# Kernel optimization log

Hardware: AMD Instinct MI355X
Metric: run time of the kernel (lower is better)

## Reference

```python
import jax, jax.numpy as jnp
import numpy as np

D_MODEL = 512
N_HEADS = 8
D_HEAD = D_MODEL // N_HEADS
B = 8
N = 1024
EPS = 1e-5  # torch LayerNorm default


def setup_inputs() -> dict:
    key = jax.random.key(0)
    ks = jax.random.split(key, 12)
    x = jax.random.normal(ks[0], (B, N, D_MODEL), dtype=jnp.float32)
    adj = (jax.random.uniform(ks[1], (B, N, N)) < 0.05).astype(jnp.float32)
    s = 1.0 / np.sqrt(D_MODEL)
    def lin(kw, kb):
        W = jax.random.uniform(kw, (D_MODEL, D_MODEL), minval=-s, maxval=s, dtype=jnp.float32)
        b = jax.random.uniform(kb, (D_MODEL,), minval=-s, maxval=s, dtype=jnp.float32)
        return W, b
    Wq, bq = lin(ks[2], ks[3])
    Wk, bk = lin(ks[4], ks[5])
    Wv, bv = lin(ks[6], ks[7])
    Wo, bo = lin(ks[8], ks[9])
    gamma = jnp.ones((D_MODEL,), dtype=jnp.float32)
    beta = jnp.zeros((D_MODEL,), dtype=jnp.float32)
    return {"x": x, "adj": adj, "Wq": Wq, "bq": bq, "Wk": Wk, "bk": bk,
            "Wv": Wv, "bv": bv, "Wo": Wo, "bo": bo, "gamma": gamma, "beta": beta}


def reference(x, adj, Wq, bq, Wk, bk, Wv, bv, Wo, bo, gamma, beta):
    Bsz, n, _ = x.shape
    # QKV projections -> [b, h, n, d]
    def proj(W, b):
        y = x @ W.T + b
        return y.reshape(Bsz, n, N_HEADS, D_HEAD).transpose(0, 2, 1, 3)
    q, k, v = proj(Wq, bq), proj(Wk, bk), proj(Wv, bv)
    scores = jnp.einsum('bhqd,bhkd->bhqk', q, k) / np.sqrt(D_HEAD)
    # adjacency mask + self-loops, broadcast over heads
    mask = (adj + jnp.eye(n, dtype=adj.dtype)[None]) > 0  # [b, n, n]
    scores = jnp.where(mask[:, None], scores, -jnp.inf)
    attn = jax.nn.softmax(scores, axis=-1)  # dropout is identity in eval
    out = jnp.einsum('bhqk,bhkd->bhqd', attn, v)
    out = out.transpose(0, 2, 1, 3).reshape(Bsz, n, D_MODEL)
    out = out @ Wo.T + bo
    # residual + LayerNorm
    h = x + out
    mu = jnp.mean(h, axis=-1, keepdims=True)
    var = jnp.mean(jnp.square(h - mu), axis=-1, keepdims=True)
    return (h - mu) * jax.lax.rsqrt(var + EPS) * gamma + beta
```

## Files before the change

### kernel.cpp

```cpp
#include <hip/hip_runtime.h>

typedef __bf16 bf16;
typedef bf16 bf16x8 __attribute__((ext_vector_type(8)));
typedef bf16 bf16x4 __attribute__((ext_vector_type(4)));
typedef bf16 bf16x2 __attribute__((ext_vector_type(2)));
typedef float f32x4 __attribute__((ext_vector_type(4)));
typedef unsigned long long u64;

#define B_SZ 8
#define N_SEQ 1024
#define DMODEL 512
#define N_HEADS 8
#define D_HEAD 64
#define M_ROWS 8192

#define QSCALE 0.18033688011112042f

static constexpr size_t OFF_XB   = 0;
static constexpr size_t OFF_WQKV = (size_t)M_ROWS * DMODEL * 2;
static constexpr size_t OFF_WO   = OFF_WQKV + (size_t)1536 * 512 * 2;
static constexpr size_t OFF_BQKV = OFF_WO + (size_t)512 * 512 * 2;
static constexpr size_t OFF_Q    = OFF_BQKV + 1536 * 4;
static constexpr size_t OFF_K    = OFF_Q + (size_t)64 * 1024 * 64 * 2;
static constexpr size_t OFF_V    = OFF_K + (size_t)64 * 1024 * 64 * 2;
static constexpr size_t OFF_MASK = OFF_V + (size_t)64 * 1024 * 64 * 2;

#define PREP_X_BLK 4096
#define PREP_W_BLK 4102
#define PREP_M_BLK 32768

__device__ __forceinline__ f32x4 mfma16(bf16x8 a, bf16x8 b, f32x4 c) {
  return __builtin_amdgcn_mfma_f32_16x16x32_bf16(a, b, c, 0, 0, 0);
}

__device__ __forceinline__ int sidx(int row, int col) {
  return (row << 6) + (col ^ ((row & 7) << 3));
}

__device__ __forceinline__ void gload16(const void* g, void* l) {
  __builtin_amdgcn_global_load_lds(
      (const __attribute__((address_space(1))) void*)g,
      (__attribute__((address_space(3))) void*)l, 16, 0, 0);
}

__global__ void k_prep(const float* __restrict__ x, const float* __restrict__ adj,
                       const float* __restrict__ Wq, const float* __restrict__ Wk,
                       const float* __restrict__ Wv, const float* __restrict__ Wo,
                       const float* __restrict__ bq, const float* __restrict__ bk,
                       const float* __restrict__ bv,
                       bf16* __restrict__ xb, bf16* __restrict__ wqkv,
                       bf16* __restrict__ wo, float* __restrict__ bqkv,
                       u64* __restrict__ maskb) {
  int b = blockIdx.x;
  if (b < PREP_X_BLK) {
    int i = b * 256 + threadIdx.x;
    float4 v = reinterpret_cast<const float4*>(x)[i];
    bf16x4 o = { (bf16)v.x, (bf16)v.y, (bf16)v.z, (bf16)v.w };
    *reinterpret_cast<bf16x4*>(xb + (size_t)i * 4) = o;
  } else if (b < PREP_X_BLK + PREP_W_BLK) {
    int tid = (b - PREP_X_BLK) * 256 + threadIdx.x;
    if (tid < 1536 * 512) {
      int row = tid >> 9;
      const float* Wsrc = row < 512 ? Wq : row < 1024 ? Wk : Wv;
      wqkv[tid] = (bf16)Wsrc[((row & 511) << 9) | (tid & 511)];
    } else if (tid < 1536 * 512 + 512 * 512) {
      int t = tid - 1536 * 512;
      wo[t] = (bf16)Wo[t];
    } else if (tid < 1536 * 512 + 512 * 512 + 1536) {
      int t = tid - (1536 * 512 + 512 * 512);
      bqkv[t] = t < 512 ? bq[t] : t < 1024 ? bk[t - 512] : bv[t - 1024];
    }
  } else {
    int idx = (b - (PREP_X_BLK + PREP_W_BLK)) * 256 + threadIdx.x;
    int q = (idx >> 10) & 1023, k = idx & 1023;
    bool pred = (adj[idx] > 0.f) || (q == k);
    u64 bal = __ballot(pred);
    if ((threadIdx.x & 63) == 0) maskb[idx >> 6] = bal;
  }
}

__global__ __launch_bounds__(256) void k_gemm(const bf16* __restrict__ A,
    const bf16* __restrict__ W, int ncols, int mode,
    const float* __restrict__ bias, const float* __restrict__ xres,
    bf16* __restrict__ oq, bf16* __restrict__ okk, bf16* __restrict__ ov,
    bf16* __restrict__ oh) {
  __shared__ bf16 Al[128 * 64];
  __shared__ bf16 Bl[128 * 64];
  int nbx = ncols >> 7;
  int bx = blockIdx.x % nbx, by = blockIdx.x / nbx;
  int m0 = by << 7, n0 = bx << 7;
  int tid = threadIdx.x, lane = tid & 63, w = tid >> 6;
  int wr = (w >> 1) << 6, wc = (w & 1) << 6;
  int lrow = lane & 15, lg = lane >> 4, lko = lg * 8;
  int rl = lane >> 3;
  int csw = ((lane & 7) ^ rl) << 3;

  const bf16* Asrc = A + (size_t)(m0 + w * 32 + rl) * DMODEL + csw;
  const bf16* Wsrc = W + (size_t)(n0 + w * 32 + rl) * DMODEL + csw;
  bf16* Adst = &Al[(w * 4) * 512];
  bf16* Bdst = &Bl[(w * 4) * 512];

  f32x4 acc[4][4];
#pragma unroll
  for (int i = 0; i < 4; i++)
#pragma unroll
    for (int j = 0; j < 4; j++) acc[i][j] = f32x4{0.f, 0.f, 0.f, 0.f};

  for (int k0 = 0; k0 < DMODEL; k0 += 64) {
    __syncthreads();
#pragma unroll
    for (int i = 0; i < 4; i++) {
      gload16(Asrc + k0 + (size_t)i * 8 * DMODEL, Adst + i * 512);
      gload16(Wsrc + k0 + (size_t)i * 8 * DMODEL, Bdst + i * 512);
    }
    __syncthreads();

    bf16x8 afr[4][2], bfr[4][2];
#pragma unroll
    for (int i = 0; i < 4; i++) {
      afr[i][0] = *reinterpret_cast<const bf16x8*>(&Al[sidx(wr + i * 16 + lrow, lko)]);
      afr[i][1] = *reinterpret_cast<const bf16x8*>(&Al[sidx(wr + i * 16 + lrow, 32 + lko)]);
      bfr[i][0] = *reinterpret_cast<const bf16x8*>(&Bl[sidx(wc + i * 16 + lrow, lko)]);
      bfr[i][1] = *reinterpret_cast<const bf16x8*>(&Bl[sidx(wc + i * 16 + lrow, 32 + lko)]);
    }
#pragma unroll
    for (int i = 0; i < 4; i++)
#pragma unroll
      for (int j = 0; j < 4; j++) {
        acc[i][j] = mfma16(afr[i][0], bfr[j][0], acc[i][j]);
        acc[i][j] = mfma16(afr[i][1], bfr[j][1], acc[i][j]);
      }
  }

  int rbase = lg * 4;
  if (mode == 0) {
#pragma unroll
    for (int i = 0; i < 4; i++) {
      int row0 = m0 + wr + i * 16 + rbase;
#pragma unroll
      for (int j = 0; j < 4; j++) {
        int col = n0 + wc + j * 16 + lrow;
        int which = col >> 9, c2 = col & 511, hh = c2 >> 6, dd = c2 & 63;
        float bi = bias[col];
        if (which == 2) {
          int bb = row0 >> 10, nn = row0 & 1023;
          bf16x4 pack;
#pragma unroll
          for (int r = 0; r < 4; r++) pack[r] = (bf16)(acc[i][j][r] + bi);
          *reinterpret_cast<bf16x4*>(
              &ov[(((size_t)bb * N_HEADS + hh) * D_HEAD + dd) * N_SEQ + nn]) = pack;
        } else {
          bf16* dst = which == 0 ? oq : okk;
          float scl = which == 0 ? QSCALE : 1.0f;
#pragma unroll
          for (int r = 0; r < 4; r++) {
            int gm = row0 + r;
            int bb = gm >> 10, nn = gm & 1023;
            dst[(((size_t)bb * N_HEADS + hh) * N_SEQ + nn) * D_HEAD + dd] =
                (bf16)((acc[i][j][r] + bi) * scl);
          }
        }
      }
    }
  } else {
#pragma unroll
    for (int i = 0; i < 4; i++) {
      int row0 = m0 + wr + i * 16 + rbase;
#pragma unroll
      for (int j = 0; j < 4; j++) {
        int col = n0 + wc + j * 16 + lrow;
        float bi = bias[col];
#pragma unroll
        for (int r = 0; r < 4; r++) {
          int gm = row0 + r;
          float y = acc[i][j][r] + bi + xres[(size_t)gm * DMODEL + col];
          oh[(size_t)gm * DMODEL + col] = (bf16)y;
        }
      }
    }
  }
}

__global__ __launch_bounds__(256, 2) void k_attn(const bf16* __restrict__ Qb,
    const bf16* __restrict__ Kb, const bf16* __restrict__ Vtg,
    const u64* __restrict__ maskb, bf16* __restrict__ attn_out) {
  __shared__ bf16 Kl[2][64 * 64];
  __shared__ bf16 Vt[2][64 * 64];
  __shared__ bf16 Pl[4][32 * 64];

  int bid = blockIdx.x;
  int work = ((bid & 7) << 6) | (bid >> 3);
  int bh = work >> 3, qb = work & 7;
  int bb = bh >> 3, hh = bh & 7;
  int tid = threadIdx.x, lane = tid & 63, w = tid >> 6;
  int lrow = lane & 15, lg = lane >> 4, lko = lg * 8;
  int rl = lane >> 3;
  int csw = ((lane & 7) ^ rl) << 3;
  int q0w = qb * 128 + w * 32;

  const bf16* Qh = Qb + (size_t)bh * N_SEQ * D_HEAD;
  const bf16* Kh = Kb + (size_t)bh * N_SEQ * D_HEAD;
  const bf16* Vh = Vtg + (size_t)bh * D_HEAD * N_SEQ;
  const u64* mrow = maskb + (size_t)bb * N_SEQ * 16;

  const bf16* Ksrc = Kh + (size_t)(w * 16 + rl) * D_HEAD + csw;
  const bf16* Vsrc = Vh + (size_t)(w * 16 + rl) * N_SEQ + csw;

  bf16x8 qf[2][2];
#pragma unroll
  for (int s = 0; s < 2; s++) {
    qf[s][0] = *reinterpret_cast<const bf16x8*>(&Qh[(q0w + s * 16 + lrow) * 64 + lko]);
    qf[s][1] = *reinterpret_cast<const bf16x8*>(&Qh[(q0w + s * 16 + lrow) * 64 + 32 + lko]);
  }

  f32x4 o[2][4];
  float ls[2][4];
#pragma unroll
  for (int s = 0; s < 2; s++)
#pragma unroll
    for (int t = 0; t < 4; t++) {
      o[s][t] = f32x4{0.f, 0.f, 0.f, 0.f};
      ls[s][t] = 0.f;
    }

#define STAGE(buf, kt0)                                                     \
  {                                                                         \
    _Pragma("unroll") for (int i = 0; i < 2; i++) {                         \
      gload16(Ksrc + (size_t)(kt0) * 64 + i * 512, &Kl[buf][(w * 2 + i) * 512]); \
      gload16(Vsrc + (size_t)i * 8192 + (kt0), &Vt[buf][(w * 2 + i) * 512]);     \
    }                                                                       \
  }

  STAGE(0, 0);
  __syncthreads();
  int cur = 0;

  for (int kt = 0; kt < 16; kt++) {
    int kt0 = kt << 6;
    u64 mw[2][4];
#pragma unroll
    for (int s = 0; s < 2; s++)
#pragma unroll
      for (int r = 0; r < 4; r++)
        mw[s][r] = mrow[(size_t)(q0w + s * 16 + lg * 4 + r) * 16 + kt];

    if (kt < 15) STAGE(cur ^ 1, kt0 + 64);

    f32x4 sc[2][4];
#pragma unroll
    for (int t = 0; t < 4; t++) {
      bf16x8 kf0 = *reinterpret_cast<const bf16x8*>(&Kl[cur][sidx(t * 16 + lrow, lko)]);
      bf16x8 kf1 = *reinterpret_cast<const bf16x8*>(&Kl[cur][sidx(t * 16 + lrow, 32 + lko)]);
#pragma unroll
      for (int s = 0; s < 2; s++) {
        sc[s][t] = f32x4{0.f, 0.f, 0.f, 0.f};
        sc[s][t] = mfma16(qf[s][0], kf0, sc[s][t]);
        sc[s][t] = mfma16(qf[s][1], kf1, sc[s][t]);
      }
    }

#pragma unroll
    for (int s = 0; s < 2; s++)
#pragma unroll
      for (int r = 0; r < 4; r++) {
#pragma unroll
        for (int t = 0; t < 4; t++) {
          bool bit = (mw[s][r] >> (t * 16 + lrow)) & 1ull;
          float pv = bit ? exp2f(sc[s][t][r]) : 0.f;
          ls[s][r] += pv;
          Pl[w][sidx(s * 16 + lg * 4 + r, t * 16 + lrow)] = (bf16)pv;
        }
      }

    bf16x8 pf[2][2];
#pragma unroll
    for (int s = 0; s < 2; s++) {
      pf[s][0] = *reinterpret_cast<const bf16x8*>(&Pl[w][sidx(s * 16 + lrow, lko)]);
      pf[s][1] = *reinterpret_cast<const bf16x8*>(&Pl[w][sidx(s * 16 + lrow, 32 + lko)]);
    }
#pragma unroll
    for (int dt = 0; dt < 4; dt++) {
      bf16x8 vf0 = *reinterpret_cast<const bf16x8*>(&Vt[cur][sidx(dt * 16 + lrow, lko)]);
      bf16x8 vf1 = *reinterpret_cast<const bf16x8*>(&Vt[cur][sidx(dt * 16 + lrow, 32 + lko)]);
#pragma unroll
      for (int s = 0; s < 2; s++) {
        o[s][dt] = mfma16(pf[s][0], vf0, o[s][dt]);
        o[s][dt] = mfma16(pf[s][1], vf1, o[s][dt]);
      }
    }

    __syncthreads();
    cur ^= 1;
  }

#pragma unroll
  for (int s = 0; s < 2; s++)
#pragma unroll
    for (int r = 0; r < 4; r++) {
      ls[s][r] += __shfl_xor(ls[s][r], 1);
      ls[s][r] += __shfl_xor(ls[s][r], 2);
      ls[s][r] += __shfl_xor(ls[s][r], 4);
      ls[s][r] += __shfl_xor(ls[s][r], 8);
    }

#pragma unroll
  for (int s = 0; s < 2; s++)
#pragma unroll
    for (int dt = 0; dt < 4; dt++) {
      int gc = hh * 64 + dt * 16 + lrow;
#pragma unroll
      for (int r = 0; r < 4; r++) {
        int gq = q0w + s * 16 + lg * 4 + r;
        float val = o[s][dt][r] / ls[s][r];
        attn_out[((size_t)(bb * N_SEQ + gq)) * DMODEL + gc] = (bf16)val;
      }
    }
#undef STAGE
}

__global__ __launch_bounds__(256) void k_ln(const bf16* __restrict__ hb,
    const float* __restrict__ gamma, const float* __restrict__ beta,
    float* __restrict__ out) {
  int row = blockIdx.x, tid = threadIdx.x;
  bf16x2 v2 = *reinterpret_cast<const bf16x2*>(hb + (size_t)row * DMODEL + tid * 2);
  float vx = (float)v2[0], vy = (float)v2[1];
  float s = vx + vy, ss = vx * vx + vy * vy;
#pragma unroll
  for (int off = 1; off < 64; off <<= 1) {
    s += __shfl_xor(s, off);
    ss += __shfl_xor(ss, off);
  }
  __shared__ float as_[4], ass_[4];
  int w = tid >> 6;
  if ((tid & 63) == 0) { as_[w] = s; ass_[w] = ss; }
  __syncthreads();
  s = as_[0] + as_[1] + as_[2] + as_[3];
  ss = ass_[0] + ass_[1] + ass_[2] + ass_[3];
  float mu = s * (1.f / 512.f);
  float var = ss * (1.f / 512.f) - mu * mu;
  float rstd = rsqrtf(var + 1e-5f);
  float2 g = reinterpret_cast<const float2*>(gamma)[tid];
  float2 bt = reinterpret_cast<const float2*>(beta)[tid];
  float2 o;
  o.x = (vx - mu) * rstd * g.x + bt.x;
  o.y = (vy - mu) * rstd * g.y + bt.y;
  reinterpret_cast<float2*>(out + (size_t)row * DMODEL)[tid] = o;
}

extern "C" void kernel_launch(void* const* d_in, const int* in_sizes, int n_in,
                              void* d_out, int out_size, void* d_ws, size_t ws_size,
                              hipStream_t stream) {
  const float* x     = (const float*)d_in[0];
  const float* adj   = (const float*)d_in[1];
  const float* Wq    = (const float*)d_in[2];
  const float* bq    = (const float*)d_in[3];
  const float* Wk    = (const float*)d_in[4];
  const float* bk    = (const float*)d_in[5];
  const float* Wv    = (const float*)d_in[6];
  const float* bv    = (const float*)d_in[7];
  const float* Wo    = (const float*)d_in[8];
  const float* bo    = (const float*)d_in[9];
  const float* gamma = (const float*)d_in[10];
  const float* beta  = (const float*)d_in[11];

  char* ws = (char*)d_ws;
  bf16* xb    = (bf16*)(ws + OFF_XB);
  bf16* wqkv  = (bf16*)(ws + OFF_WQKV);
  bf16* wo    = (bf16*)(ws + OFF_WO);
  float* bqkv = (float*)(ws + OFF_BQKV);
  bf16* Qb    = (bf16*)(ws + OFF_Q);
  bf16* Kb    = (bf16*)(ws + OFF_K);
  bf16* Vb    = (bf16*)(ws + OFF_V);
  u64* maskb  = (u64*)(ws + OFF_MASK);
  bf16* attn  = xb;
  bf16* hb    = (bf16*)(ws + OFF_Q);
  float* out  = (float*)d_out;

  k_prep<<<dim3(PREP_X_BLK + PREP_W_BLK + PREP_M_BLK), dim3(256), 0, stream>>>(
      x, adj, Wq, Wk, Wv, Wo, bq, bk, bv, xb, wqkv, wo, bqkv, maskb);

  k_gemm<<<dim3((M_ROWS / 128) * (1536 / 128)), dim3(256), 0, stream>>>(
      xb, wqkv, 1536, 0, bqkv, nullptr, Qb, Kb, Vb, nullptr);

  k_attn<<<dim3(512), dim3(256), 0, stream>>>(Qb, Kb, Vb, maskb, attn);

  k_gemm<<<dim3((M_ROWS / 128) * (512 / 128)), dim3(256), 0, stream>>>(
      attn, wo, 512, 1, bo, x, nullptr, nullptr, nullptr, hb);

  k_ln<<<dim3(M_ROWS), dim3(256), 0, stream>>>(hb, gamma, beta, out);
}
```

Baseline: 116.3 us.

## Split attention keys across waves and reduce partial outputs in shared memory

The attention kernel now gives each block 32 queries instead of 128 and launches four times as many blocks. The four waves split each 64-key tile, each taking 16 keys, instead of splitting queries. K and V are read straight from global memory and no longer staged through double-buffered LDS. Scores are computed transposed, so the probabilities land in registers already in MFMA operand layout, which removes the per-tile P round trip through LDS and the per-tile block barrier. Partial outputs are reduced across waves through shared memory at the end. The costs are extra global loads with half-empty bf16x8 MFMA operands for V, and a bf16 rounding of the partial outputs before the reduction.

```diff
diff --git a/kernel.cpp b/kernel.cpp
--- a/kernel.cpp
+++ b/kernel.cpp
@@ -181,141 +181,112 @@
   }
 }
 
-__global__ __launch_bounds__(256, 2) void k_attn(const bf16* __restrict__ Qb,
+__global__ __launch_bounds__(256, 4) void k_attn(const bf16* __restrict__ Qb,
     const bf16* __restrict__ Kb, const bf16* __restrict__ Vtg,
     const u64* __restrict__ maskb, bf16* __restrict__ attn_out) {
-  __shared__ bf16 Kl[2][64 * 64];
-  __shared__ bf16 Vt[2][64 * 64];
-  __shared__ bf16 Pl[4][32 * 64];
+  __shared__ bf16 Op[4][64][36];
+  __shared__ float lsp[4][32];
 
   int bid = blockIdx.x;
-  int work = ((bid & 7) << 6) | (bid >> 3);
-  int bh = work >> 3, qb = work & 7;
+  int work = ((bid & 7) << 8) | (bid >> 3);
+  int bh = work >> 5, qb = work & 31;
   int bb = bh >> 3, hh = bh & 7;
   int tid = threadIdx.x, lane = tid & 63, w = tid >> 6;
-  int lrow = lane & 15, lg = lane >> 4, lko = lg * 8;
-  int rl = lane >> 3;
-  int csw = ((lane & 7) ^ rl) << 3;
-  int q0w = qb * 128 + w * 32;
+  int lrow = lane & 15, lg = lane >> 4;
+  int q0blk = qb * 32;
 
   const bf16* Qh = Qb + (size_t)bh * N_SEQ * D_HEAD;
   const bf16* Kh = Kb + (size_t)bh * N_SEQ * D_HEAD;
   const bf16* Vh = Vtg + (size_t)bh * D_HEAD * N_SEQ;
   const u64* mrow = maskb + (size_t)bb * N_SEQ * 16;
 
-  const bf16* Ksrc = Kh + (size_t)(w * 16 + rl) * D_HEAD + csw;
-  const bf16* Vsrc = Vh + (size_t)(w * 16 + rl) * N_SEQ + csw;
-
   bf16x8 qf[2][2];
 #pragma unroll
   for (int s = 0; s < 2; s++) {
-    qf[s][0] = *reinterpret_cast<const bf16x8*>(&Qh[(q0w + s * 16 + lrow) * 64 + lko]);
-    qf[s][1] = *reinterpret_cast<const bf16x8*>(&Qh[(q0w + s * 16 + lrow) * 64 + 32 + lko]);
+    qf[s][0] = *reinterpret_cast<const bf16x8*>(&Qh[(q0blk + s * 16 + lrow) * 64 + lg * 8]);
+    qf[s][1] = *reinterpret_cast<const bf16x8*>(&Qh[(q0blk + s * 16 + lrow) * 64 + 32 + lg * 8]);
   }
 
   f32x4 o[2][4];
-  float ls[2][4];
 #pragma unroll
   for (int s = 0; s < 2; s++)
 #pragma unroll
-    for (int t = 0; t < 4; t++) {
-      o[s][t] = f32x4{0.f, 0.f, 0.f, 0.f};
-      ls[s][t] = 0.f;
-    }
-
-#define STAGE(buf, kt0)                                                     \
-  {                                                                         \
-    _Pragma("unroll") for (int i = 0; i < 2; i++) {                         \
-      gload16(Ksrc + (size_t)(kt0) * 64 + i * 512, &Kl[buf][(w * 2 + i) * 512]); \
-      gload16(Vsrc + (size_t)i * 8192 + (kt0), &Vt[buf][(w * 2 + i) * 512]);     \
-    }                                                                       \
-  }
-
-  STAGE(0, 0);
+    for (int d = 0; d < 4; d++) o[s][d] = f32x4{0.f, 0.f, 0.f, 0.f};
+  float ls0 = 0.f, ls1 = 0.f;
+
+  int mbit = w * 16 + lg * 4;
+
+  for (int kt = 0; kt < 16; kt++) {
+    int krow = kt * 64 + w * 16 + lrow;
+    bf16x8 kf0 = *reinterpret_cast<const bf16x8*>(&Kh[(size_t)krow * 64 + lg * 8]);
+    bf16x8 kf1 = *reinterpret_cast<const bf16x8*>(&Kh[(size_t)krow * 64 + 32 + lg * 8]);
+    u64 mw0 = mrow[(size_t)(q0blk + lrow) * 16 + kt];
+    u64 mw1 = mrow[(size_t)(q0blk + 16 + lrow) * 16 + kt];
+
+    f32x4 sc0 = f32x4{0.f, 0.f, 0.f, 0.f}, sc1 = f32x4{0.f, 0.f, 0.f, 0.f};
+    sc0 = mfma16(kf0, qf[0][0], sc0);
+    sc0 = mfma16(kf1, qf[0][1], sc0);
+    sc1 = mfma16(kf0, qf[1][0], sc1);
+    sc1 = mfma16(kf1, qf[1][1], sc1);
+
+    bf16x8 pa0 = {}, pa1 = {};
+#pragma unroll
+    for (int r = 0; r < 4; r++) {
+      float p0 = ((mw0 >> (mbit + r)) & 1ull) ? exp2f(sc0[r]) : 0.f;
+      float p1 = ((mw1 >> (mbit + r)) & 1ull) ? exp2f(sc1[r]) : 0.f;
+      ls0 += p0;
+      ls1 += p1;
+      pa0[r] = (bf16)p0;
+      pa1[r] = (bf16)p1;
+    }
+
+#pragma unroll
+    for (int d = 0; d < 4; d++) {
+      bf16x4 v4 = *reinterpret_cast<const bf16x4*>(
+          &Vh[(size_t)(d * 16 + lrow) * N_SEQ + kt * 64 + w * 16 + lg * 4]);
+      bf16x8 vf = {v4[0], v4[1], v4[2], v4[3],
+                   (bf16)0.f, (bf16)0.f, (bf16)0.f, (bf16)0.f};
+      o[0][d] = mfma16(pa0, vf, o[0][d]);
+      o[1][d] = mfma16(pa1, vf, o[1][d]);
+    }
+  }
+
+  ls0 += __shfl_xor(ls0, 16); ls0 += __shfl_xor(ls0, 32);
+  ls1 += __shfl_xor(ls1, 16); ls1 += __shfl_xor(ls1, 32);
+  if (lane < 16) {
+    lsp[w][lrow] = ls0;
+    lsp[w][16 + lrow] = ls1;
+  }
+
+#pragma unroll
+  for (int s = 0; s < 2; s++)
+#pragma unroll
+    for (int d = 0; d < 4; d++) {
+      bf16x4 pk;
+#pragma unroll
+      for (int r = 0; r < 4; r++) pk[r] = (bf16)o[s][d][r];
+      *reinterpret_cast<bf16x4*>(&Op[w][d * 16 + lrow][s * 16 + lg * 4]) = pk;
+    }
   __syncthreads();
-  int cur = 0;
-
-  for (int kt = 0; kt < 16; kt++) {
-    int kt0 = kt << 6;
-    u64 mw[2][4];
-#pragma unroll
-    for (int s = 0; s < 2; s++)
-#pragma unroll
-      for (int r = 0; r < 4; r++)
-        mw[s][r] = mrow[(size_t)(q0w + s * 16 + lg * 4 + r) * 16 + kt];
-
-    if (kt < 15) STAGE(cur ^ 1, kt0 + 64);
-
-    f32x4 sc[2][4];
-#pragma unroll
-    for (int t = 0; t < 4; t++) {
-      bf16x8 kf0 = *reinterpret_cast<const bf16x8*>(&Kl[cur][sidx(t * 16 + lrow, lko)]);
-      bf16x8 kf1 = *reinterpret_cast<const bf16x8*>(&Kl[cur][sidx(t * 16 + lrow, 32 + lko)]);
-#pragma unroll
-      for (int s = 0; s < 2; s++) {
-        sc[s][t] = f32x4{0.f, 0.f, 0.f, 0.f};
-        sc[s][t] = mfma16(qf[s][0], kf0, sc[s][t]);
-        sc[s][t] = mfma16(qf[s][1], kf1, sc[s][t]);
-      }
-    }
-
-#pragma unroll
-    for (int s = 0; s < 2; s++)
-#pragma unroll
-      for (int r = 0; r < 4; r++) {
-#pragma unroll
-        for (int t = 0; t < 4; t++) {
-          bool bit = (mw[s][r] >> (t * 16 + lrow)) & 1ull;
-          float pv = bit ? exp2f(sc[s][t][r]) : 0.f;
-          ls[s][r] += pv;
-          Pl[w][sidx(s * 16 + lg * 4 + r, t * 16 + lrow)] = (bf16)pv;
-        }
-      }
-
-    bf16x8 pf[2][2];
-#pragma unroll
-    for (int s = 0; s < 2; s++) {
-      pf[s][0] = *reinterpret_cast<const bf16x8*>(&Pl[w][sidx(s * 16 + lrow, lko)]);
-      pf[s][1] = *reinterpret_cast<const bf16x8*>(&Pl[w][sidx(s * 16 + lrow, 32 + lko)]);
-    }
-#pragma unroll
-    for (int dt = 0; dt < 4; dt++) {
-      bf16x8 vf0 = *reinterpret_cast<const bf16x8*>(&Vt[cur][sidx(dt * 16 + lrow, lko)]);
-      bf16x8 vf1 = *reinterpret_cast<const bf16x8*>(&Vt[cur][sidx(dt * 16 + lrow, 32 + lko)]);
-#pragma unroll
-      for (int s = 0; s < 2; s++) {
-        o[s][dt] = mfma16(pf[s][0], vf0, o[s][dt]);
-        o[s][dt] = mfma16(pf[s][1], vf1, o[s][dt]);
-      }
-    }
-
-    __syncthreads();
-    cur ^= 1;
-  }
-
-#pragma unroll
-  for (int s = 0; s < 2; s++)
+
+#pragma unroll
+  for (int s = 0; s < 2; s++) {
+    f32x4 sum = f32x4{0.f, 0.f, 0.f, 0.f};
+#pragma unroll
+    for (int wv = 0; wv < 4; wv++) {
+      bf16x4 rp = *reinterpret_cast<const bf16x4*>(&Op[wv][w * 16 + lrow][s * 16 + lg * 4]);
+#pragma unroll
+      for (int r = 0; r < 4; r++) sum[r] += (float)rp[r];
+    }
 #pragma unroll
     for (int r = 0; r < 4; r++) {
-      ls[s][r] += __shfl_xor(ls[s][r], 1);
-      ls[s][r] += __shfl_xor(ls[s][r], 2);
-      ls[s][r] += __shfl_xor(ls[s][r], 4);
-      ls[s][r] += __shfl_xor(ls[s][r], 8);
-    }
-
-#pragma unroll
-  for (int s = 0; s < 2; s++)
-#pragma unroll
-    for (int dt = 0; dt < 4; dt++) {
-      int gc = hh * 64 + dt * 16 + lrow;
-#pragma unroll
-      for (int r = 0; r < 4; r++) {
-        int gq = q0w + s * 16 + lg * 4 + r;
-        float val = o[s][dt][r] / ls[s][r];
-        attn_out[((size_t)(bb * N_SEQ + gq)) * DMODEL + gc] = (bf16)val;
-      }
-    }
-#undef STAGE
+      int q = s * 16 + lg * 4 + r;
+      float lsq = lsp[0][q] + lsp[1][q] + lsp[2][q] + lsp[3][q];
+      int gq = q0blk + q;
+      attn_out[((size_t)(bb * N_SEQ + gq)) * DMODEL + hh * 64 + w * 16 + lrow] =
+          (bf16)(sum[r] / lsq);
+    }
+  }
 }
 
 __global__ __launch_bounds__(256) void k_ln(const bf16* __restrict__ hb,
@@ -382,7 +353,7 @@
   k_gemm<<<dim3((M_ROWS / 128) * (1536 / 128)), dim3(256), 0, stream>>>(
       xb, wqkv, 1536, 0, bqkv, nullptr, Qb, Kb, Vb, nullptr);
 
-  k_attn<<<dim3(512), dim3(256), 0, stream>>>(Qb, Kb, Vb, maskb, attn);
+  k_attn<<<dim3(2048), dim3(256), 0, stream>>>(Qb, Kb, Vb, maskb, attn);
 
   k_gemm<<<dim3((M_ROWS / 128) * (512 / 128)), dim3(256), 0, stream>>>(
       attn, wo, 512, 1, bo, x, nullptr, nullptr, nullptr, hb);
```

Measured after the change: 188.3 us. 61.9% more time.
